# Kernel tuning notes

Measured on AMD Instinct MI355X. Metric: run time of the kernel, lower is better.

Reference implementation:

```python
import jax, jax.numpy as jnp
import numpy as np

EPS = 1e-5
DIM = 32          # head_dim
HEADS = 8         # in_channels // dim * heads_ratio = 256 // 32

def hardswish(x):
    return x * jnp.clip(x + 3.0, 0.0, 6.0) / 6.0

def conv1x1(x, w):
    # w: (C_out, C_in); x: (B, C_in, H, W)
    return jnp.einsum('oi,bihw->bohw', w, x)

def dwconv(x, w, pad):
    # depthwise conv, w: (C, 1, kh, kw)
    return jax.lax.conv_general_dilated(
        x, w, (1, 1), [(pad, pad), (pad, pad)],
        dimension_numbers=('NCHW', 'OIHW', 'NCHW'),
        feature_group_count=x.shape[1])

def gconv1x1(x, w, groups):
    # grouped 1x1 conv, w: (C_out, C_in//groups, 1, 1)
    return jax.lax.conv_general_dilated(
        x, w, (1, 1), [(0, 0), (0, 0)],
        dimension_numbers=('NCHW', 'OIHW', 'NCHW'),
        feature_group_count=groups)


def setup_inputs() -> dict:
    key = jax.random.key(0)
    ks = jax.random.split(key, 12)
    B, C, H, W = 16, 256, 32, 32
    td = HEADS * DIM          # 256 (total_dim per branch)
    c3 = 3 * td               # 768
    mid = 4 * C               # 1024 (expand_ratio=4)

    def rn(k, shape, fan_in):
        return jax.random.normal(k, shape, jnp.float32) * (1.0 / np.sqrt(fan_in))

    return {
        'x': jax.random.normal(ks[0], (B, C, H, W), jnp.float32),
        # LiteMLA
        'w_qkv': rn(ks[1], (c3, C), C),                 # 1x1, bias=False, no norm
        'w_agg_dw': rn(ks[2], (c3, 1, 5, 5), 25),       # depthwise 5x5, pad 2
        'w_agg_pw': rn(ks[3], (c3, DIM, 1, 1), DIM),    # grouped 1x1, groups=3*HEADS
        'w_proj': rn(ks[4], (C, 2 * td), 2 * td),       # 1x1, bias=False (BN follows)
        'bn_proj_scale': jnp.ones((C,), jnp.float32) + 0.1 * jax.random.normal(ks[5], (C,), jnp.float32),
        'bn_proj_bias': 0.1 * jax.random.normal(ks[6], (C,), jnp.float32),
        # MBConv
        'w_mb1': rn(ks[7], (mid, C), C),
        'b_mb1': jnp.zeros((mid,), jnp.float32),
        'w_mb_dw': rn(ks[8], (mid, 1, 3, 3), 9),
        'b_mb_dw': jnp.zeros((mid,), jnp.float32),
        'w_mb2': rn(ks[9], (C, mid), mid),              # bias=False (BN follows)
        'bn2_scale': jnp.ones((C,), jnp.float32) + 0.1 * jax.random.normal(ks[10], (C,), jnp.float32),
        'bn2_bias': 0.1 * jax.random.normal(ks[11], (C,), jnp.float32),
    }


def reference(x, w_qkv, w_agg_dw, w_agg_pw, w_proj, bn_proj_scale, bn_proj_bias,
              w_mb1, b_mb1, w_mb_dw, b_mb_dw, w_mb2, bn2_scale, bn2_bias):
    B, C, H, W = x.shape
    # ---- LiteMLA context module (residual) ----
    qkv = conv1x1(x, w_qkv)                                   # (B, 768, H, W)
    agg = gconv1x1(dwconv(qkv, w_agg_dw, 2), w_agg_pw, 3 * HEADS)
    ms = jnp.concatenate([qkv, agg], axis=1)                  # (B, 1536, H, W)
    nh = ms.shape[1] // (3 * DIM)                             # 16 total heads
    t = ms.reshape(B, nh, 3 * DIM, H * W).transpose(0, 1, 3, 2)  # (B, nh, HW, 3*DIM)
    q, k, v = jnp.split(t, 3, axis=-1)                        # each (B, nh, HW, DIM)
    q = jax.nn.relu(q).astype(jnp.float32)
    k = jax.nn.relu(k).astype(jnp.float32)
    v = jnp.pad(v.astype(jnp.float32), ((0, 0), (0, 0), (0, 0), (0, 1)),
                constant_values=1.0)                          # (B, nh, HW, DIM+1)
    kv = jnp.einsum('bhnd,bhne->bhde', k, v)                  # (B, nh, DIM, DIM+1)
    out = jnp.einsum('bhnd,bhde->bhne', q, kv)                # (B, nh, HW, DIM+1)
    out = out[..., :-1] / (out[..., -1:] + EPS)
    out = out.astype(x.dtype)
    out = out.transpose(0, 1, 3, 2).reshape(B, nh * DIM, H, W)  # (B, 512, H, W)
    out = conv1x1(out, w_proj)
    out = out * bn_proj_scale[:, None, None] + bn_proj_bias[:, None, None]
    x = x + out                                               # residual
    # ---- MBConv local module (residual) ----
    h = hardswish(conv1x1(x, w_mb1) + b_mb1[:, None, None])
    h = hardswish(dwconv(h, w_mb_dw, 1) + b_mb_dw[:, None, None])
    h = conv1x1(h, w_mb2)
    h = h * bn2_scale[:, None, None] + bn2_bias[:, None, None]
    return x + h
```

## Files before the change

kernel.cpp:

```cpp
#include <hip/hip_runtime.h>
#include <hip/hip_bf16.h>


typedef unsigned short u16;
typedef __attribute__((ext_vector_type(8))) short short8;
typedef __attribute__((ext_vector_type(4))) short short4v;
typedef __attribute__((ext_vector_type(4))) float f32x4;

#define HW 1024
#define EPSV 1e-5f
#define MFMA16(a, b, c) __builtin_amdgcn_mfma_f32_16x16x32_bf16((a), (b), (c), 0, 0, 0)
#define FB(n) ((((n) ^ ((n) >> 3))) & 7)

__device__ __forceinline__ u16 f2bf(float f) {
    union { __hip_bfloat16 h; u16 u; } c; c.h = __float2bfloat16(f); return c.u;
}
__device__ __forceinline__ float bf2f(u16 u) {
    union { u16 u; __hip_bfloat16 h; } c; c.u = u; return __bfloat162float(c.h);
}
__device__ __forceinline__ float hswish(float v) {
    return v * fminf(fmaxf(v + 3.f, 0.f), 6.f) * (1.f / 6.f);
}
__device__ __forceinline__ void gload_lds16(const u16* g, u16* lds) {
    __builtin_amdgcn_global_load_lds(
        (const __attribute__((address_space(1))) void*)g,
        (__attribute__((address_space(3))) void*)lds, 16, 0, 0);
}

__global__ __launch_bounds__(256) void prep_k(
    const float* __restrict__ x,  u16* __restrict__ xb,
    const float* __restrict__ wq, u16* __restrict__ wqb,
    const float* __restrict__ wp, u16* __restrict__ wpb,
    const float* __restrict__ w1, u16* __restrict__ w1b,
    const float* __restrict__ w2, u16* __restrict__ w2b)
{
    const int N0 = 4194304, N1 = 196608, N2 = 131072, N3 = 262144;
    const int total = N0 + N1 + N2 + N3 + 262144;
    for (int i = blockIdx.x * 256 + threadIdx.x; i < total; i += gridDim.x * 256) {
        int id = i;
        if (id < N0) { xb[id]  = f2bf(x[id]);  continue; } id -= N0;
        if (id < N1) { wqb[id] = f2bf(wq[id]); continue; } id -= N1;
        if (id < N2) { wpb[id] = f2bf(wp[id]); continue; } id -= N2;
        if (id < N3) { w1b[id] = f2bf(w1[id]); continue; } id -= N3;
        w2b[id] = f2bf(w2[id]);
    }
}

template<int EPI, int TM>
__global__ __launch_bounds__(TM * 2) void gemm_bf(
    const u16* __restrict__ A, const u16* __restrict__ Bact,
    const float* __restrict__ s1, const float* __restrict__ s2,
    const float* __restrict__ Rres, float* __restrict__ outF,
    u16* __restrict__ outB, int M, int K)
{
    constexpr int NW = TM / 32;
    constexpr int NT = TM * 2;
    constexpr int NQ = 256 / NT;
    constexpr int ABUF = TM * 64;
    constexpr int BBUF = 128 * 64;
    const int b  = blockIdx.z;
    const int n0 = blockIdx.x * 128;
    const int m0 = blockIdx.y * TM;
    const int t  = threadIdx.x;
    const int l  = t & 63, w = t >> 6;
    const int lr = t & 15, lg = (t >> 4) & 3;
    const int wm = (TM == 128) ? (w >> 1) : 0;
    const int wn = (TM == 128) ? (w & 1) : w;

    __shared__ __attribute__((aligned(16))) u16 As[2 * ABUF];
    __shared__ __attribute__((aligned(16))) u16 Bs[2 * BBUF];

    const u16* Ab0 = A + (size_t)m0 * K;
    const u16* Bp  = Bact + (size_t)b * K * HW + n0;

    int brow[4], bfb[4];
    #pragma unroll
    for (int j = 0; j < 4; ++j) {
        brow[j] = wn * 64 + j * 16 + lr;
        bfb[j]  = FB(brow[j]);
    }

    short4v breg[NQ][8];

    auto issueA = [&](int k0, int sel) {
        u16* dst = As + (size_t)sel * ABUF;
        #pragma unroll
        for (int u = 0; u < 4; ++u) {
            int g = (u * NW + w) * 64 + l;
            int row = g >> 3, cl = g & 7;
            int cs = cl ^ (row & 7);
            gload_lds16(Ab0 + (size_t)row * K + k0 + cs * 8,
                        dst + (size_t)(u * NW + w) * 512);
        }
    };
    auto loadB = [&](int k0) {
        #pragma unroll
        for (int q = 0; q < NQ; ++q) {
            const int kc = (t >> 5) + q * (NT / 32);
            const int n4 = t & 31;
            #pragma unroll
            for (int kk = 0; kk < 8; ++kk)
                breg[q][kk] = *(const short4v*)(Bp + (size_t)(k0 + kc * 8 + kk) * HW + n4 * 4);
        }
    };
    auto writeB = [&](int sel) {
        u16* dst = Bs + (size_t)sel * BBUF;
        #pragma unroll
        for (int q = 0; q < NQ; ++q) {
            const int kc = (t >> 5) + q * (NT / 32);
            const int n4 = t & 31;
            #pragma unroll
            for (int nn = 0; nn < 4; ++nn) {
                const int n = n4 * 4 + nn;
                short8 wv = { breg[q][0][nn], breg[q][1][nn], breg[q][2][nn],
                              breg[q][3][nn], breg[q][4][nn], breg[q][5][nn],
                              breg[q][6][nn], breg[q][7][nn] };
                *(short8*)(&dst[n * 64 + ((kc ^ FB(n)) * 8)]) = wv;
            }
        }
    };

    f32x4 zero4 = {0.f, 0.f, 0.f, 0.f};
    f32x4 acc[4][4];
    #pragma unroll
    for (int i = 0; i < 4; ++i)
        #pragma unroll
        for (int j = 0; j < 4; ++j) acc[i][j] = zero4;

    const int ntk = K >> 6;
    issueA(0, 0);
    loadB(0);
    writeB(0);
    __syncthreads();

    int cur = 0;
    for (int tile = 0; tile < ntk; ++tile) {
        const int nxt = cur ^ 1;
        const bool pf = (tile + 1 < ntk);
        if (pf) { issueA((tile + 1) << 6, nxt); loadB((tile + 1) << 6); }

        const u16* Asb = As + (size_t)cur * ABUF;
        const u16* Bsb = Bs + (size_t)cur * BBUF;
        #pragma unroll
        for (int kk = 0; kk < 2; ++kk) {
            short8 a[4], bb[4];
            #pragma unroll
            for (int i = 0; i < 4; ++i) {
                int row = wm * 64 + i * 16 + lr;
                a[i] = *(const short8*)(&Asb[row * 64 + (((kk * 4 + lg) ^ (lr & 7)) * 8)]);
            }
            #pragma unroll
            for (int j = 0; j < 4; ++j)
                bb[j] = *(const short8*)(&Bsb[brow[j] * 64 + (((kk * 4 + lg) ^ bfb[j]) * 8)]);
            #pragma unroll
            for (int i = 0; i < 4; ++i)
                #pragma unroll
                for (int j = 0; j < 4; ++j)
                    acc[i][j] = MFMA16(a[i], bb[j], acc[i][j]);
        }
        if (pf) writeB(nxt);
        __syncthreads();
        cur = nxt;
    }

    const size_t obase = (size_t)b * M * HW;
    #pragma unroll
    for (int i = 0; i < 4; ++i) {
        #pragma unroll
        for (int r = 0; r < 4; ++r) {
            const int grow = m0 + wm * 64 + i * 16 + lg * 4 + r;
            float p1 = 0.f, p2 = 0.f;
            if (EPI == 1) { p1 = s1[grow]; }
            if (EPI >= 2) { p1 = s1[grow]; p2 = s2[grow]; }
            #pragma unroll
            for (int j = 0; j < 4; ++j) {
                const int gcol = n0 + wn * 64 + j * 16 + lr;
                const size_t off = obase + (size_t)grow * HW + gcol;
                float v = acc[i][j][r];
                if (EPI == 0) { outB[off] = f2bf(v); }
                if (EPI == 1) { v = hswish(v + p1); outB[off] = f2bf(v); }
                if (EPI == 2) { v = v * p1 + p2 + Rres[off]; outF[off] = v; outB[off] = f2bf(v); }
                if (EPI == 3) { v = v * p1 + p2 + Rres[off]; outF[off] = v; }
            }
        }
    }
}

template<int KS, int PAD, int NCH, bool HS>
__global__ __launch_bounds__(256) void dwconv_k(
    const u16* __restrict__ in, const float* __restrict__ w,
    const float* __restrict__ bias, u16* __restrict__ out)
{
    constexpr int T = 32 + 2 * PAD;
    __shared__ float tile[T * T];
    const int plane = blockIdx.x;
    const int c = plane % NCH;
    const u16* ip = in + (size_t)plane * HW;
    const int t = threadIdx.x;
    for (int idx = t; idx < T * T; idx += 256) {
        int r = idx / T, cc = idx % T;
        int gr = r - PAD, gc = cc - PAD;
        float v = 0.f;
        if ((unsigned)gr < 32u && (unsigned)gc < 32u) v = bf2f(ip[gr * 32 + gc]);
        tile[idx] = v;
    }
    float wl[KS * KS];
    #pragma unroll
    for (int u = 0; u < KS * KS; ++u) wl[u] = w[c * KS * KS + u];
    const float bv = HS ? bias[c] : 0.f;
    __syncthreads();
    #pragma unroll
    for (int pj = 0; pj < 4; ++pj) {
        const int px = t + pj * 256;
        const int pr = px >> 5, pc = px & 31;
        float s = bv;
        #pragma unroll
        for (int dr = 0; dr < KS; ++dr)
            #pragma unroll
            for (int dc = 0; dc < KS; ++dc)
                s += tile[(pr + dr) * T + pc + dc] * wl[dr * KS + dc];
        if (HS) s = hswish(s);
        out[(size_t)plane * HW + px] = f2bf(s);
    }
}

__global__ __launch_bounds__(256) void gconv_k(
    const u16* __restrict__ dw, const float* __restrict__ wpw,
    u16* __restrict__ agg)
{
    const int gx = blockIdx.x;
    const int g = gx >> 2, nt = gx & 3;
    const int b = blockIdx.y;
    const int n0 = nt * 256;
    const int t = threadIdx.x;
    __shared__ float dt[32][256];
    __shared__ float wl[32 * 32];
    const u16* dp = dw + ((size_t)b * 768 + g * 32) * HW + n0;
    for (int idx = t; idx < 32 * 256; idx += 256) {
        int i = idx >> 8, nn = idx & 255;
        dt[i][nn] = bf2f(dp[(size_t)i * HW + nn]);
    }
    for (int idx = t; idx < 1024; idx += 256) wl[idx] = wpw[g * 1024 + idx];
    __syncthreads();
    float acc[32] = {};
    #pragma unroll
    for (int i = 0; i < 32; ++i) {
        const float d = dt[i][t];
        #pragma unroll
        for (int oc = 0; oc < 32; ++oc) acc[oc] += wl[oc * 32 + i] * d;
    }
    u16* ap = agg + ((size_t)b * 768 + g * 32) * HW + n0;
    #pragma unroll
    for (int oc = 0; oc < 32; ++oc) ap[(size_t)oc * HW + t] = f2bf(acc[oc]);
}

__global__ __launch_bounds__(64) void kv_k(
    const u16* __restrict__ qkvb, const u16* __restrict__ aggb,
    float* __restrict__ kvp)
{
    const int blk = blockIdx.x;
    const int bh = blk >> 2, nc = blk & 3;
    const int b = bh >> 4, h = bh & 15;
    const u16* src = (h < 8) ? qkvb + ((size_t)b * 768 + h * 96) * HW
                             : aggb + ((size_t)b * 768 + (h - 8) * 96) * HW;
    const u16* kp = src + 32 * HW + nc * 256;
    const u16* vp = src + 64 * HW + nc * 256;
    const int l = threadIdx.x;
    const int lr = l & 15, lg = l >> 4;

    f32x4 zero4 = {0.f, 0.f, 0.f, 0.f};
    f32x4 acc[2][3];
    #pragma unroll
    for (int i = 0; i < 2; ++i)
        #pragma unroll
        for (int j = 0; j < 3; ++j) acc[i][j] = zero4;

    short8 bones;
    #pragma unroll
    for (int g = 0; g < 8; ++g) bones[g] = (lr == 0) ? (short)0x3F80 : (short)0;

    for (int ks = 0; ks < 8; ++ks) {
        const int kn = ks * 32 + lg * 8;
        short8 a0 = *(const short8*)(kp + (size_t)lr * HW + kn);
        short8 a1 = *(const short8*)(kp + (size_t)(16 + lr) * HW + kn);
        #pragma unroll
        for (int g = 0; g < 8; ++g) {
            if (((u16)a0[g]) & 0x8000) a0[g] = 0;
            if (((u16)a1[g]) & 0x8000) a1[g] = 0;
        }
        short8 b0 = *(const short8*)(vp + (size_t)lr * HW + kn);
        short8 b1 = *(const short8*)(vp + (size_t)(16 + lr) * HW + kn);
        acc[0][0] = MFMA16(a0, b0, acc[0][0]);
        acc[0][1] = MFMA16(a0, b1, acc[0][1]);
        acc[0][2] = MFMA16(a0, bones, acc[0][2]);
        acc[1][0] = MFMA16(a1, b0, acc[1][0]);
        acc[1][1] = MFMA16(a1, b1, acc[1][1]);
        acc[1][2] = MFMA16(a1, bones, acc[1][2]);
    }
    float* dst = kvp + (size_t)blk * 1056;
    #pragma unroll
    for (int dt = 0; dt < 2; ++dt)
        #pragma unroll
        for (int et = 0; et < 3; ++et)
            #pragma unroll
            for (int r = 0; r < 4; ++r) {
                const int d = dt * 16 + lg * 4 + r;
                const int e = et * 16 + lr;
                if (et < 2 || lr == 0) dst[d * 33 + e] = acc[dt][et][r];
            }
}

__global__ __launch_bounds__(256) void attn_k(
    const u16* __restrict__ qkvb, const u16* __restrict__ aggb,
    const float* __restrict__ kvp, u16* __restrict__ attnb)
{
    const int blk = blockIdx.x;
    const int bh = blk >> 2, nc = blk & 3;
    const int b = bh >> 4, h = bh & 15;
    const u16* qp = (h < 8) ? qkvb + ((size_t)b * 768 + h * 96) * HW
                            : aggb + ((size_t)b * 768 + (h - 8) * 96) * HW;
    __shared__ u16 qs[256 * 40];
    const int t = threadIdx.x;
    #pragma unroll 4
    for (int u = 0; u < 32; ++u) {
        int id = t + u * 256;
        int d = id >> 8, n = id & 255;
        u16 q = qp[(size_t)d * HW + nc * 256 + n];
        if (q & 0x8000) q = 0;
        qs[n * 40 + d] = q;
    }
    const int lr = t & 15, lg = (t >> 4) & 3, w = t >> 6;

    short8 bf[3];
    const float* kb = kvp + (size_t)bh * 4 * 1056;
    #pragma unroll
    for (int et = 0; et < 3; ++et)
        #pragma unroll
        for (int j = 0; j < 8; ++j) {
            const int d = lg * 8 + j, e = et * 16 + lr;
            float s = 0.f;
            if (e <= 32) {
                #pragma unroll
                for (int c = 0; c < 4; ++c) s += kb[c * 1056 + d * 33 + e];
            }
            bf[et][j] = (short)f2bf(s);
        }
    __syncthreads();

    f32x4 zero4 = {0.f, 0.f, 0.f, 0.f};
    f32x4 acc[4][3];
    #pragma unroll
    for (int i = 0; i < 4; ++i) {
        const int row = w * 64 + i * 16 + lr;
        short8 a = *(const short8*)(&qs[row * 40 + lg * 8]);
        #pragma unroll
        for (int et = 0; et < 3; ++et) acc[i][et] = MFMA16(a, bf[et], zero4);
    }

    u16* ap = attnb + (size_t)b * 512 * HW + (size_t)h * 32 * HW;
    #pragma unroll
    for (int i = 0; i < 4; ++i) {
        float inv[4];
        #pragma unroll
        for (int r = 0; r < 4; ++r) {
            const float den = __shfl(acc[i][2][r], t & 48, 64);
            inv[r] = 1.f / (den + EPSV);
        }
        const int nbase = nc * 256 + w * 64 + i * 16 + lg * 4;
        #pragma unroll
        for (int et = 0; et < 2; ++et) {
            const int e = et * 16 + lr;
            short4v o;
            #pragma unroll
            for (int r = 0; r < 4; ++r) o[r] = (short)f2bf(acc[i][et][r] * inv[r]);
            *(short4v*)(ap + (size_t)e * HW + nbase) = o;
        }
    }
}

extern "C" void kernel_launch(void* const* d_in, const int* in_sizes, int n_in,
                              void* d_out, int out_size, void* d_ws, size_t ws_size,
                              hipStream_t stream)
{
    const float* x        = (const float*)d_in[0];
    const float* w_qkv    = (const float*)d_in[1];
    const float* w_agg_dw = (const float*)d_in[2];
    const float* w_agg_pw = (const float*)d_in[3];
    const float* w_proj   = (const float*)d_in[4];
    const float* bnp_s    = (const float*)d_in[5];
    const float* bnp_b    = (const float*)d_in[6];
    const float* w_mb1    = (const float*)d_in[7];
    const float* b_mb1    = (const float*)d_in[8];
    const float* w_mb_dw  = (const float*)d_in[9];
    const float* b_mb_dw  = (const float*)d_in[10];
    const float* w_mb2    = (const float*)d_in[11];
    const float* bn2_s    = (const float*)d_in[12];
    const float* bn2_b    = (const float*)d_in[13];
    float* out = (float*)d_out;
    char*  W   = (char*)d_ws;

    u16*   qkvb  = (u16*)(W + 0);
    u16*   xb    = (u16*)(W + 25165824);
    u16*   dwb   = (u16*)(W + 33554432);
    u16*   aggb  = (u16*)(W + 58720256);
    float* kvp   = (float*)(W + 83886080);
    u16*   attnb = (u16*)(W + 33554432);
    u16*   h1b   = (u16*)(W + 0);
    u16*   h2b   = (u16*)(W + 58720256);
    float* y1f   = (float*)(W + 92274688);
    u16*   y1b   = (u16*)(W + 109051904);
    u16*   wqb   = (u16*)(W + 117440512);
    u16*   wpb   = (u16*)(W + 117833728);
    u16*   w1b   = (u16*)(W + 118095872);
    u16*   w2b   = (u16*)(W + 118620160);

    prep_k<<<2048, 256, 0, stream>>>(x, xb, w_qkv, wqb, w_proj, wpb,
                                     w_mb1, w1b, w_mb2, w2b);
    gemm_bf<0, 128><<<dim3(8, 6, 16), 256, 0, stream>>>(
        wqb, xb, nullptr, nullptr, nullptr, nullptr, qkvb, 768, 256);
    dwconv_k<5, 2, 768, false><<<dim3(16 * 768), 256, 0, stream>>>(
        qkvb, w_agg_dw, nullptr, dwb);
    gconv_k<<<dim3(96, 16), 256, 0, stream>>>(dwb, w_agg_pw, aggb);
    kv_k<<<dim3(1024), 64, 0, stream>>>(qkvb, aggb, kvp);
    attn_k<<<dim3(1024), 256, 0, stream>>>(qkvb, aggb, kvp, attnb);
    gemm_bf<2, 64><<<dim3(8, 4, 16), 128, 0, stream>>>(
        wpb, attnb, bnp_s, bnp_b, x, y1f, y1b, 256, 512);
    gemm_bf<1, 128><<<dim3(8, 8, 16), 256, 0, stream>>>(
        w1b, y1b, b_mb1, nullptr, nullptr, nullptr, h1b, 1024, 256);
    dwconv_k<3, 1, 1024, true><<<dim3(16 * 1024), 256, 0, stream>>>(
        h1b, w_mb_dw, b_mb_dw, h2b);
    gemm_bf<3, 64><<<dim3(8, 4, 16), 128, 0, stream>>>(
        w2b, h2b, bn2_s, bn2_b, y1f, out, nullptr, 256, 1024);
}
```

Measured before the change: 266.3 us.

## Read GEMM A operand from global directly; register-tile depthwise conv 2x2 outputs

The GEMM no longer stages the weight (A) tile into LDS through global_load_lds. Each wave now reads its A fragments straight from global memory, relying on cache reuse and freeing LDS for occupancy. Separately, the depthwise conv has each thread compute a 2x2 output block from a register window, cutting LDS reads and writing packed bf16 pairs. The risk is that uncoalesced, unprefetched global loads of A sit on the MFMA critical path.

```diff
diff --git a/kernel.cpp b/kernel.cpp
--- a/kernel.cpp
+++ b/kernel.cpp
@@ -5,6 +5,7 @@
 typedef unsigned short u16;
 typedef __attribute__((ext_vector_type(8))) short short8;
 typedef __attribute__((ext_vector_type(4))) short short4v;
+typedef __attribute__((ext_vector_type(2))) short short2v;
 typedef __attribute__((ext_vector_type(4))) float f32x4;
 
 #define HW 1024
@@ -20,11 +21,6 @@
 }
 __device__ __forceinline__ float hswish(float v) {
     return v * fminf(fmaxf(v + 3.f, 0.f), 6.f) * (1.f / 6.f);
-}
-__device__ __forceinline__ void gload_lds16(const u16* g, u16* lds) {
-    __builtin_amdgcn_global_load_lds(
-        (const __attribute__((address_space(1))) void*)g,
-        (__attribute__((address_space(3))) void*)lds, 16, 0, 0);
 }
 
 __global__ __launch_bounds__(256) void prep_k(
@@ -56,18 +52,16 @@
     constexpr int NW = TM / 32;
     constexpr int NT = TM * 2;
     constexpr int NQ = 256 / NT;
-    constexpr int ABUF = TM * 64;
     constexpr int BBUF = 128 * 64;
     const int b  = blockIdx.z;
     const int n0 = blockIdx.x * 128;
     const int m0 = blockIdx.y * TM;
     const int t  = threadIdx.x;
-    const int l  = t & 63, w = t >> 6;
+    const int w  = t >> 6;
     const int lr = t & 15, lg = (t >> 4) & 3;
     const int wm = (TM == 128) ? (w >> 1) : 0;
     const int wn = (TM == 128) ? (w & 1) : w;
 
-    __shared__ __attribute__((aligned(16))) u16 As[2 * ABUF];
     __shared__ __attribute__((aligned(16))) u16 Bs[2 * BBUF];
 
     const u16* Ab0 = A + (size_t)m0 * K;
@@ -82,17 +76,6 @@
 
     short4v breg[NQ][8];
 
-    auto issueA = [&](int k0, int sel) {
-        u16* dst = As + (size_t)sel * ABUF;
-        #pragma unroll
-        for (int u = 0; u < 4; ++u) {
-            int g = (u * NW + w) * 64 + l;
-            int row = g >> 3, cl = g & 7;
-            int cs = cl ^ (row & 7);
-            gload_lds16(Ab0 + (size_t)row * K + k0 + cs * 8,
-                        dst + (size_t)(u * NW + w) * 512);
-        }
-    };
     auto loadB = [&](int k0) {
         #pragma unroll
         for (int q = 0; q < NQ; ++q) {
@@ -128,7 +111,6 @@
         for (int j = 0; j < 4; ++j) acc[i][j] = zero4;
 
     const int ntk = K >> 6;
-    issueA(0, 0);
     loadB(0);
     writeB(0);
     __syncthreads();
@@ -137,9 +119,9 @@
     for (int tile = 0; tile < ntk; ++tile) {
         const int nxt = cur ^ 1;
         const bool pf = (tile + 1 < ntk);
-        if (pf) { issueA((tile + 1) << 6, nxt); loadB((tile + 1) << 6); }
-
-        const u16* Asb = As + (size_t)cur * ABUF;
+        if (pf) loadB((tile + 1) << 6);
+
+        const int k0 = tile << 6;
         const u16* Bsb = Bs + (size_t)cur * BBUF;
         #pragma unroll
         for (int kk = 0; kk < 2; ++kk) {
@@ -147,7 +129,7 @@
             #pragma unroll
             for (int i = 0; i < 4; ++i) {
                 int row = wm * 64 + i * 16 + lr;
-                a[i] = *(const short8*)(&Asb[row * 64 + (((kk * 4 + lg) ^ (lr & 7)) * 8)]);
+                a[i] = *(const short8*)(Ab0 + (size_t)row * K + k0 + kk * 32 + lg * 8);
             }
             #pragma unroll
             for (int j = 0; j < 4; ++j)
@@ -192,6 +174,7 @@
     const float* __restrict__ bias, u16* __restrict__ out)
 {
     constexpr int T = 32 + 2 * PAD;
+    constexpr int WN = KS + 1;
     __shared__ float tile[T * T];
     const int plane = blockIdx.x;
     const int c = plane % NCH;
@@ -209,18 +192,29 @@
     for (int u = 0; u < KS * KS; ++u) wl[u] = w[c * KS * KS + u];
     const float bv = HS ? bias[c] : 0.f;
     __syncthreads();
-    #pragma unroll
-    for (int pj = 0; pj < 4; ++pj) {
-        const int px = t + pj * 256;
-        const int pr = px >> 5, pc = px & 31;
-        float s = bv;
+
+    const int tx = t & 15, ty = t >> 4;
+    float win[WN][WN];
+    #pragma unroll
+    for (int dr = 0; dr < WN; ++dr)
+        #pragma unroll
+        for (int dc = 0; dc < WN; ++dc)
+            win[dr][dc] = tile[(2 * ty + dr) * T + 2 * tx + dc];
+
+    #pragma unroll
+    for (int i = 0; i < 2; ++i) {
+        float s0 = bv, s1 = bv;
         #pragma unroll
         for (int dr = 0; dr < KS; ++dr)
             #pragma unroll
-            for (int dc = 0; dc < KS; ++dc)
-                s += tile[(pr + dr) * T + pc + dc] * wl[dr * KS + dc];
-        if (HS) s = hswish(s);
-        out[(size_t)plane * HW + px] = f2bf(s);
+            for (int dc = 0; dc < KS; ++dc) {
+                const float wv = wl[dr * KS + dc];
+                s0 += win[i + dr][0 + dc] * wv;
+                s1 += win[i + dr][1 + dc] * wv;
+            }
+        if (HS) { s0 = hswish(s0); s1 = hswish(s1); }
+        short2v o = { (short)f2bf(s0), (short)f2bf(s1) };
+        *(short2v*)(out + (size_t)plane * HW + (2 * ty + i) * 32 + 2 * tx) = o;
     }
 }
 
```

Result: slower. 293.3 us (+10.1%).
